# Kernel tuning notes

Hardware: AMD Instinct MI355X
Metric: run time of the kernel (lower is better)

The kernel has to match this reference:

```python
import jax, jax.numpy as jnp
import numpy as np
from jax.scipy.linalg import cho_solve

N, D, K, M = 2048, 128, 8, 64
JITTER = 1e-5


def setup_inputs() -> dict:
    key = jax.random.key(0)
    ks = jax.random.split(key, 5)
    X = jax.random.normal(ks[0], (N, D), jnp.float32)
    Y = jax.random.normal(ks[1], (N, 1), jnp.float32)
    q_mu = 0.1 * jax.random.normal(ks[2], (K, D), jnp.float32)
    # positive variational covariances ~ 1/D, as in the original init
    q_cov = jax.random.uniform(ks[3], (K, D), jnp.float32, 0.5 / D, 1.5 / D)
    Z = jax.random.normal(ks[4], (M, K), jnp.float32)
    sigma_f = jnp.float32(1.0)
    noise_var = jnp.float32(0.01)
    return {"X": X, "Y": Y, "q_mu": q_mu, "q_cov": q_cov, "Z": Z,
            "sigma_f": sigma_f, "noise_var": noise_var}


def _compute_psi1(X, q_mu, q_cov, Z, sigma_f):
    # q_mu_X: (K, N)
    q_mu_X = jnp.einsum('kd,nd->kn', q_mu, X)
    # top: (K, N, M)
    top = (q_mu_X[:, :, None] - Z.T[:, None, :]) ** 2
    # bot: (K, N)
    bot = 1.0 + jnp.einsum('kd,nd->kn', q_cov, X * X)
    bot = bot[:, :, None]
    psi1 = jnp.exp(-0.5 * top / bot) / jnp.sqrt(bot)  # (K, N, M)
    return sigma_f * jnp.prod(psi1, axis=0)  # (N, M)


def _compute_batched_psi2(X, q_mu, q_cov, Z, sigma_f):
    q_mu_X = jnp.einsum('kd,nd->kn', q_mu, X)  # (K, N)
    Z_diff = Z[:, None, :] - Z[None, :, :]      # (M, M, K)
    Z_bar = 0.5 * (Z[:, None, :] + Z[None, :, :])  # (M, M, K)
    # top: (K, N, M, M) -- the dominant intermediate
    top = (q_mu_X[:, :, None, None] - jnp.transpose(Z_bar, (2, 0, 1))[:, None, :, :]) ** 2
    bot = 2.0 * jnp.einsum('kd,nd->kn', q_cov, X * X) + 1.0  # (K, N)
    bot = bot[:, :, None, None]
    right = jnp.prod(jnp.exp(-top / bot) / jnp.sqrt(bot), axis=0)  # (N, M, M)
    left = (sigma_f ** 2) * jnp.exp(-0.25 * jnp.sum(Z_diff ** 2, axis=2))  # (M, M)
    return left * right  # (N, M, M)


def _rbf_K(Z):
    # ARD RBF with unit variance and unit lengthscales (frozen in original)
    sq = jnp.sum((Z[:, None, :] - Z[None, :, :]) ** 2, axis=-1)
    return jnp.exp(-0.5 * sq)


def _chol_logdet(chol):
    return 2.0 * jnp.sum(jnp.log(jnp.diagonal(chol)), axis=-1)


def _elbo(X, Y, q_mu, q_cov, Z, sigma_f, noise_var):
    n = X.shape[0]
    d = X.shape[1]
    m = Z.shape[0]
    sigma2 = jnp.reshape(noise_var, ())
    sf = jnp.reshape(sigma_f, ())
    two_pi = jnp.asarray(2.0 * np.pi, X.dtype)
    eye = jnp.eye(m, dtype=X.dtype)

    Kuu = _rbf_K(Z) + eye * JITTER
    chol_Ku = jnp.linalg.cholesky(Kuu)
    F1 = -n * jnp.log(two_pi) - (n - m) * jnp.log(sigma2) + _chol_logdet(chol_Ku)

    YY = Y.T @ Y  # (1, 1)
    psi2 = jnp.sum(_compute_batched_psi2(X, q_mu, q_cov, Z, sf), axis=0)  # (M, M)
    Ku_Psi2 = sigma2 * Kuu + psi2 + eye * JITTER
    chol_Ku_Psi2 = jnp.linalg.cholesky(Ku_Psi2)
    F1 = F1 - _chol_logdet(chol_Ku_Psi2) - YY / sigma2  # (1, 1)

    psi1 = _compute_psi1(X, q_mu, q_cov, Z, sf)  # (N, M)
    Psi1_Y = psi1.T @ Y  # (M, 1)
    F1 = F1 + (Psi1_Y.T @ cho_solve((chol_Ku_Psi2, True), Psi1_Y)) / sigma2

    psi0 = n * sf ** 2
    KuiPsi2 = cho_solve((chol_Ku, True), psi2)
    F1 = F1 - psi0 / sigma2 + jnp.trace(KuiPsi2) / sigma2

    KL = jnp.sum(jnp.log(q_cov), axis=1)
    KL = KL - d * jnp.log(jnp.sum(q_cov + q_mu ** 2, axis=1))
    KL = KL + d * jnp.asarray(np.log(d), X.dtype)
    KL = jnp.sum(KL)
    return jnp.squeeze(0.5 * (F1 + KL))


def reference(X, Y, q_mu, q_cov, Z, sigma_f, noise_var):
    return _elbo(X, Y, q_mu, q_cov, Z, sigma_f, noise_var)
```

## Files before the change

### kernel.cpp

```cpp
#include <hip/hip_runtime.h>
#include <math.h>

namespace {
constexpr int N_ = 2048;
constexpr int D_ = 128;
constexpr int K_ = 8;
constexpr int M_ = 64;
constexpr float JIT = 1e-5f;
constexpr float L2E = 1.4426950408889634f;
constexpr float LN2 = 0.6931471805599453f;

constexpr int OFF_ARR2 = 16;
constexpr int OFF_C2   = OFF_ARR2 + N_ * 16;
constexpr int OFF_ARR1 = OFF_C2 + N_;
constexpr int OFF_CY   = OFF_ARR1 + N_ * 16;
constexpr int OFF_P2P  = OFF_CY + N_;
constexpr int OFF_P1Y  = OFF_P2P + 16 * 4096;
constexpr int OFF_PSI2 = OFF_P1Y + 512;
constexpr int OFF_KUI  = OFF_PSI2 + 4096;
constexpr int OFF_SC   = OFF_KUI + 4096;
}

struct F8 { float f[8]; };

__device__ __forceinline__ void bar_arrive(int* c) {
  __syncthreads();
  if (threadIdx.x == 0) { __threadfence(); atomicAdd(c, 1); }
}
__device__ __forceinline__ void bar_wait(int* c, int target) {
  if (threadIdx.x == 0) {
    while (__hip_atomic_load(c, __ATOMIC_RELAXED, __HIP_MEMORY_SCOPE_AGENT) < target)
      __builtin_amdgcn_s_sleep(16);
    __threadfence();
  }
  __syncthreads();
}

__device__ __forceinline__ float sweep2x2_w4(
    float* reg, float (*rowbuf)[2][M_], int wave, int lane) {
  float ld = 0.f;
#pragma unroll
  for (int p = 0; p < M_; p += 2) {
    const int par = (p >> 1) & 1;
    float* rbA = rowbuf[par][0];
    float* rbB = rowbuf[par][1];
    const int rp = p & 15;
    if (wave == (p >> 4)) {
      rbA[lane] = reg[rp];
      rbB[lane] = reg[rp + 1];
    }
    __syncthreads();

    const float P00 = rbA[p];
    const float P01 = rbA[p + 1];
    const float P11 = rbB[p + 1];
    const float a0  = rbA[lane];
    const float a1  = rbB[lane];
    const float det = fmaf(P00, P11, -P01 * P01);
    const float idet = __builtin_amdgcn_rcpf(det);
    ld += __log2f(det);
    const float Pi00 =  P11 * idet;
    const float Pi01 = -P01 * idet;
    const float Pi11 =  P00 * idet;

    const bool isp = (lane == p), isq = (lane == p + 1);
    const float w0 = isp ? Pi00 : (isq ? Pi01 : fmaf(Pi00, a0, Pi01 * a1));
    const float w1 = isp ? Pi01 : (isq ? Pi11 : fmaf(Pi01, a0, Pi11 * a1));
    const float t0 = isp ? (1.f - w0) : (isq ? -w0 : w0);
    const float t1 = isq ? (1.f - w1) : (isp ? -w1 : w1);
    const float f0 = (isp || isq) ? -w0 : w0;
    const float f1 = (isp || isq) ? -w1 : w1;

    const float4* rAq = reinterpret_cast<const float4*>(rbA + 16 * wave);
    const float4* rBq = reinterpret_cast<const float4*>(rbB + 16 * wave);
#pragma unroll
    for (int q = 0; q < 4; q++) {
      const float4 va = rAq[q], vb = rBq[q];
      reg[4 * q + 0] = fmaf(-t1, vb.x, fmaf(-t0, va.x, reg[4 * q + 0]));
      reg[4 * q + 1] = fmaf(-t1, vb.y, fmaf(-t0, va.y, reg[4 * q + 1]));
      reg[4 * q + 2] = fmaf(-t1, vb.z, fmaf(-t0, va.z, reg[4 * q + 2]));
      reg[4 * q + 3] = fmaf(-t1, vb.w, fmaf(-t0, va.w, reg[4 * q + 3]));
    }
    if (wave == (p >> 4)) {
      reg[rp]     = f0;
      reg[rp + 1] = f1;
    }
  }
  return ld;
}

__global__ __launch_bounds__(256) void vdmgp_k1(
    const float* __restrict__ X, const float* __restrict__ Y,
    const float* __restrict__ qmu, const float* __restrict__ qcov,
    const float* __restrict__ Z, float* __restrict__ ws) {
  __shared__ float smu[D_ * K_];
  __shared__ float scov[D_ * K_];
  __shared__ float zl[M_][9];
  __shared__ __align__(16) float rowbuf[2][2][M_];
  const int tid = threadIdx.x;
  const int b = blockIdx.x;

  if (b == 0 && tid < 4) ((int*)ws)[tid] = 0;

  if (b == 8) {
    for (int idx = tid; idx < M_ * K_; idx += 256) zl[idx >> 3][idx & 7] = Z[idx];
    __syncthreads();
    const int lane = tid & 63;
    const int wave = tid >> 6;
    float zj[K_];
#pragma unroll
    for (int k = 0; k < K_; k++) zj[k] = zl[lane][k];
    float reg[16];
#pragma unroll
    for (int r = 0; r < 16; r++) {
      const int gi = 16 * wave + r;
      float sq = 0.f;
#pragma unroll
      for (int k = 0; k < K_; k++) { const float dd = zl[gi][k] - zj[k]; sq = fmaf(dd, dd, sq); }
      reg[r] = exp2f(-0.5f * L2E * sq) + ((gi == lane) ? JIT : 0.f);
    }
    const float ld1 = sweep2x2_w4(reg, rowbuf, wave, lane);
#pragma unroll
    for (int r = 0; r < 16; r++)
      ws[OFF_KUI + (16 * wave + r) * 64 + lane] = reg[r];
    if (tid == 0) ws[OFF_SC + 2] = LN2 * ld1;
    return;
  }

  if (b == 9) {
    const int lane = tid & 63;
    const int wave = tid >> 6;
    if (wave == 0) {
      float yy = 0.f;
#pragma unroll
      for (int t = 0; t < 32; t++) {
        const float y = Y[t * 64 + lane];
        yy = fmaf(y, y, yy);
      }
#pragma unroll
      for (int off = 32; off > 0; off >>= 1) yy += __shfl_down(yy, off, 64);
      if (lane == 0) ws[OFF_SC + 0] = yy;
    } else if (wave == 1) {
      const int k = lane >> 3;
      const int d0 = (lane & 7) * 16;
      float slog = 0.f, srow = 0.f;
#pragma unroll
      for (int t = 0; t < 16; t++) {
        const float qc = qcov[k * D_ + d0 + t];
        const float qm = qmu[k * D_ + d0 + t];
        slog += logf(qc);
        srow += qc + qm * qm;
      }
#pragma unroll
      for (int off = 4; off > 0; off >>= 1) {
        slog += __shfl_down(slog, off, 8);
        srow += __shfl_down(srow, off, 8);
      }
      float klr = ((lane & 7) == 0)
          ? (slog - (float)D_ * logf(srow) + (float)D_ * logf((float)D_)) : 0.f;
      klr += __shfl_down(klr, 32, 64);
      klr += __shfl_down(klr, 16, 64);
      klr += __shfl_down(klr, 8, 64);
      if (lane == 0) ws[OFF_SC + 1] = klr;
    }
    return;
  }

  for (int idx = tid; idx < K_ * D_; idx += 256) {
    int k = idx >> 7, d = idx & 127;
    smu[d * K_ + k]  = qmu[idx];
    scov[d * K_ + k] = qcov[idx];
  }
  __syncthreads();

  const int n = b * 256 + tid;
  float a[K_], s2[K_];
#pragma unroll
  for (int k = 0; k < K_; k++) { a[k] = 0.f; s2[k] = 0.f; }

  const float4* xrow = reinterpret_cast<const float4*>(X + n * D_);
#pragma unroll 2
  for (int dq = 0; dq < D_ / 4; dq++) {
    float4 xv = xrow[dq];
    float xs[4] = {xv.x, xv.y, xv.z, xv.w};
#pragma unroll
    for (int t = 0; t < 4; t++) {
      const int d = dq * 4 + t;
      const float x = xs[t];
      const float xx = x * x;
      F8 mu = *reinterpret_cast<const F8*>(&smu[d * K_]);
      F8 cv = *reinterpret_cast<const F8*>(&scov[d * K_]);
#pragma unroll
      for (int k = 0; k < K_; k++) {
        a[k]  = fmaf(mu.f[k], x, a[k]);
        s2[k] = fmaf(cv.f[k], xx, s2[k]);
      }
    }
  }

  float4 w2[4], w1[4];
  float prod2 = 1.f, prod1 = 1.f;
#pragma unroll
  for (int k = 0; k < K_; k++) {
    const float b2 = 2.f * s2[k] + 1.f;
    const float b1 = 1.f + s2[k];
    reinterpret_cast<float*>(w2)[k]     = a[k];
    reinterpret_cast<float*>(w2)[8 + k] = L2E / b2;
    reinterpret_cast<float*>(w1)[k]     = a[k];
    reinterpret_cast<float*>(w1)[8 + k] = 0.5f * L2E / b1;
    prod2 *= rsqrtf(b2);
    prod1 *= rsqrtf(b1);
  }
  float4* a2q = reinterpret_cast<float4*>(ws + OFF_ARR2 + n * 16);
  float4* a1q = reinterpret_cast<float4*>(ws + OFF_ARR1 + n * 16);
#pragma unroll
  for (int e = 0; e < 4; e++) { a2q[e] = w2[e]; a1q[e] = w1[e]; }
  (ws + OFF_C2)[n] = prod2;
  (ws + OFF_CY)[n] = prod1 * Y[n];
}

__global__ __launch_bounds__(256) void vdmgp_k2(
    const float* __restrict__ Z,
    const float* __restrict__ sfp, const float* __restrict__ nvp,
    float* __restrict__ ws, float* __restrict__ out) {
  __shared__ __align__(16) float pool[5520];

  int* bar = (int*)ws;
  const int tid = threadIdx.x;
  const int b = blockIdx.x;
  const float sf = sfp[0];

  if (b > 0) {
    const int t = b - 1;
    {
      float* sa = pool;
      float* sc = pool + 2048;
      const int chunk = t >> 4;
      const int nbase = chunk * 128;
      const float4* src = reinterpret_cast<const float4*>(ws + OFF_ARR2 + nbase * 16);
      float4* dst = reinterpret_cast<float4*>(sa);
      for (int idx = tid; idx < 128 * 4; idx += 256) dst[idx] = src[idx];
      if (tid < 128) sc[tid] = (ws + OFF_C2)[nbase + tid];
      __syncthreads();

      const int pair = (t & 15) * 256 + tid;
      const int i = pair >> 6, j = pair & 63;
      float zb[K_];
#pragma unroll
      for (int k = 0; k < K_; k++) zb[k] = 0.5f * (Z[i * K_ + k] + Z[j * K_ + k]);

      float acc = 0.f;
      for (int nl = 0; nl < 128; nl++) {
        const F8 av = *reinterpret_cast<const F8*>(&sa[nl * 16]);
        const F8 ib = *reinterpret_cast<const F8*>(&sa[nl * 16 + 8]);
        float s = 0.f;
#pragma unroll
        for (int k = 0; k < K_; k++) {
          const float tt = av.f[k] - zb[k];
          s = fmaf(tt * tt, ib.f[k], s);
        }
        acc = fmaf(sc[nl], exp2f(-s), acc);
      }
      (ws + OFF_P2P)[chunk * 4096 + pair] = acc;
    }
    bar_arrive(&bar[0]);

    if (t < 16) {
      bar_wait(&bar[0], 256);
      const int p = t * 256 + tid;
      float acc = 0.f;
#pragma unroll
      for (int c = 0; c < 16; c++) acc += ws[OFF_P2P + c * 4096 + p];
      const int i = p >> 6, j = p & 63;
      float sq = 0.f;
#pragma unroll
      for (int k = 0; k < K_; k++) {
        const float dd = Z[i * K_ + k] - Z[j * K_ + k];
        sq = fmaf(dd, dd, sq);
      }
      ws[OFF_PSI2 + p] = sf * sf * exp2f(-0.25f * L2E * sq) * acc;
      bar_arrive(&bar[2]);
    } else if (t < 24) {
      float* sa1 = pool;
      float* scy = pool + 4096;
      float* red = pool + 4352;
      const int chunk = t - 16;
      const int nbase = chunk * 256;
      const float4* src = reinterpret_cast<const float4*>(ws + OFF_ARR1 + nbase * 16);
      float4* dst = reinterpret_cast<float4*>(sa1);
#pragma unroll
      for (int r = 0; r < 4; r++) dst[r * 256 + tid] = src[r * 256 + tid];
      scy[tid] = (ws + OFF_CY)[nbase + tid];
      __syncthreads();

      const int m = tid & 63;
      const int stripe = tid >> 6;
      float zm[K_];
#pragma unroll
      for (int k = 0; k < K_; k++) zm[k] = Z[m * K_ + k];

      float acc = 0.f;
      for (int u = 0; u < 64; u++) {
        const int nl = stripe * 64 + u;
        const F8 av = *reinterpret_cast<const F8*>(&sa1[nl * 16]);
        const F8 ib = *reinterpret_cast<const F8*>(&sa1[nl * 16 + 8]);
        float s = 0.f;
#pragma unroll
        for (int k = 0; k < K_; k++) {
          const float d = av.f[k] - zm[k];
          s = fmaf(d * d, ib.f[k], s);
        }
        acc = fmaf(scy[nl], exp2f(-s), acc);
      }
      red[tid] = acc;
      __syncthreads();
      if (tid < 64)
        (ws + OFF_P1Y)[chunk * 64 + tid] =
            red[tid] + red[64 + tid] + red[128 + tid] + red[192 + tid];
      bar_arrive(&bar[1]);
    }
    return;
  }

  float (*P2s)[M_]       = reinterpret_cast<float(*)[M_]>(pool);
  float (*zl)[9]         = reinterpret_cast<float(*)[9]>(pool + 4096);
  float (*rowbuf)[2][M_] = reinterpret_cast<float(*)[2][M_]>(pool + 4672);
  float* pysL  = pool + 4928;
  float* scalL = pool + 4992;
  float* redQ  = pool + 5000;
  float* redT  = pool + 5256;

  const int lane = tid & 63;
  const int wave = tid >> 6;
  const float s2v = nvp[0];

  for (int idx = tid; idx < M_ * K_; idx += 256) zl[idx >> 3][idx & 7] = Z[idx];

  bar_wait(&bar[2], 16);
  {
    const float4* srcq = reinterpret_cast<const float4*>(ws + OFF_PSI2);
    float4* dstq = reinterpret_cast<float4*>(&P2s[0][0]);
#pragma unroll
    for (int q = 0; q < 4; q++) dstq[q * 256 + tid] = srcq[q * 256 + tid];
  }
  bar_wait(&bar[1], 8);
  if (tid < M_) {
    float s = 0.f;
#pragma unroll
    for (int c = 0; c < 8; c++) s += ws[OFF_P1Y + c * M_ + tid];
    pysL[tid] = sf * s;
  }
  __syncthreads();

  float zj[K_];
#pragma unroll
  for (int k = 0; k < K_; k++) zj[k] = zl[lane][k];
  float reg[16];
#pragma unroll
  for (int r = 0; r < 16; r++) {
    const int gi = 16 * wave + r;
    float sq = 0.f;
#pragma unroll
    for (int k = 0; k < K_; k++) { const float dd = zl[gi][k] - zj[k]; sq = fmaf(dd, dd, sq); }
    const float jit = (gi == lane) ? JIT : 0.f;
    const float kj = exp2f(-0.5f * L2E * sq) + jit;
    reg[r] = fmaf(s2v, kj, P2s[gi][lane] + jit);
  }

  const float ld2 = sweep2x2_w4(reg, rowbuf, wave, lane);

  float sQ = 0.f, sT = 0.f;
  const float* kui = ws + OFF_KUI;
#pragma unroll
  for (int r = 0; r < 16; r++) {
    const int gi = 16 * wave + r;
    sQ = fmaf(reg[r], pysL[gi], sQ);
    sT = fmaf(kui[gi * 64 + lane], P2s[gi][lane], sT);
  }
  redQ[tid] = sQ;
  redT[tid] = sT;
  if (tid == 0) scalL[6] = LN2 * ld2;
  __syncthreads();

  if (wave == 0) {
    float c = redQ[lane] + redQ[64 + lane] + redQ[128 + lane] + redQ[192 + lane];
    float q = c * pysL[lane];
#pragma unroll
    for (int off = 32; off > 0; off >>= 1) q += __shfl_down(q, off, 64);
    if (lane == 0) scalL[7] = -q;
  } else if (wave == 1) {
    float s = redT[lane] + redT[64 + lane] + redT[128 + lane] + redT[192 + lane];
#pragma unroll
    for (int off = 32; off > 0; off >>= 1) s += __shfl_down(s, off, 64);
    if (lane == 0) scalL[5] = -s;
  }
  __syncthreads();

  if (tid == 0) {
    const float YY  = ws[OFF_SC + 0];
    const float KL  = ws[OFF_SC + 1];
    const float ld1 = ws[OFF_SC + 2];
    const float tr = scalL[5], ld2v = scalL[6], quad = scalL[7];
    const float inv = 1.0f / s2v;
    const float F1 = -(float)N_ * 1.8378770664093453f
                   - (float)(N_ - M_) * logf(s2v)
                   + (ld1 - ld2v)
                   - YY * inv
                   + quad * inv
                   - (float)N_ * sf * sf * inv
                   + tr * inv;
    out[0] = 0.5f * (F1 + KL);
  }
}

extern "C" void kernel_launch(void* const* d_in, const int* in_sizes, int n_in,
                              void* d_out, int out_size, void* d_ws, size_t ws_size,
                              hipStream_t stream) {
  const float* X    = (const float*)d_in[0];
  const float* Y    = (const float*)d_in[1];
  const float* qmu  = (const float*)d_in[2];
  const float* qcov = (const float*)d_in[3];
  const float* Z    = (const float*)d_in[4];
  const float* sfp  = (const float*)d_in[5];
  const float* nvp  = (const float*)d_in[6];
  float* ws  = (float*)d_ws;
  float* out = (float*)d_out;

  vdmgp_k1<<<10, 256, 0, stream>>>(X, Y, qmu, qcov, Z, ws);
  vdmgp_k2<<<257, 256, 0, stream>>>(Z, sfp, nvp, ws, out);
}
```

Before: 52.51 us.

## Pipeline Cholesky sweep rows, split psi2 barriers, and reorder final-block waits

The 2x2 block sweep now computes the next pivot row pair early and writes it to the alternate row buffer, so each step needs one block barrier instead of two phases. The single global psi2 barrier becomes sixteen per-tile counters, so each reducer block waits only on its own sixteen producers, and the sleep intervals are shorter. The final block does its Kuu and Kui loads before waiting on psi2, reads psi2 straight from global memory instead of staging it in shared memory, and waits for psi1·Y only after the sweep. The psi2 inner loop is unrolled by four to expose more independent exp work, at the cost of more registers.

```diff
diff --git a/kernel.cpp b/kernel.cpp
--- a/kernel.cpp
+++ b/kernel.cpp
@@ -10,7 +10,7 @@
 constexpr float L2E = 1.4426950408889634f;
 constexpr float LN2 = 0.6931471805599453f;
 
-constexpr int OFF_ARR2 = 16;
+constexpr int OFF_ARR2 = 32;
 constexpr int OFF_C2   = OFF_ARR2 + N_ * 16;
 constexpr int OFF_ARR1 = OFF_C2 + N_;
 constexpr int OFF_CY   = OFF_ARR1 + N_ * 16;
@@ -27,29 +27,34 @@
   __syncthreads();
   if (threadIdx.x == 0) { __threadfence(); atomicAdd(c, 1); }
 }
+template <int SLP>
 __device__ __forceinline__ void bar_wait(int* c, int target) {
   if (threadIdx.x == 0) {
     while (__hip_atomic_load(c, __ATOMIC_RELAXED, __HIP_MEMORY_SCOPE_AGENT) < target)
-      __builtin_amdgcn_s_sleep(16);
+      __builtin_amdgcn_s_sleep(SLP);
     __threadfence();
   }
   __syncthreads();
 }
 
-__device__ __forceinline__ float sweep2x2_w4(
+__device__ __forceinline__ float sweep2x2_pipe(
     float* reg, float (*rowbuf)[2][M_], int wave, int lane) {
+  if (wave == 0) {
+    rowbuf[0][0][lane] = reg[0];
+    rowbuf[0][1][lane] = reg[1];
+  }
+  __syncthreads();
   float ld = 0.f;
 #pragma unroll
-  for (int p = 0; p < M_; p += 2) {
-    const int par = (p >> 1) & 1;
+  for (int s = 0; s < 32; ++s) {
+    const int p = 2 * s;
+    const int par = s & 1;
     float* rbA = rowbuf[par][0];
     float* rbB = rowbuf[par][1];
-    const int rp = p & 15;
-    if (wave == (p >> 4)) {
-      rbA[lane] = reg[rp];
-      rbB[lane] = reg[rp + 1];
-    }
-    __syncthreads();
+    const int own_s  = s >> 3;
+    const int own_s1 = (s + 1) >> 3;
+    const int rp  = p & 15;
+    const int rp2 = (p + 2) & 15;
 
     const float P00 = rbA[p];
     const float P01 = rbA[p + 1];
@@ -71,6 +76,13 @@
     const float f0 = (isp || isq) ? -w0 : w0;
     const float f1 = (isp || isq) ? -w1 : w1;
 
+    if (s < 31 && wave == own_s1) {
+      const float e0 = fmaf(-t1, rbB[p + 2], fmaf(-t0, rbA[p + 2], reg[rp2]));
+      const float e1 = fmaf(-t1, rbB[p + 3], fmaf(-t0, rbA[p + 3], reg[rp2 + 1]));
+      rowbuf[par ^ 1][0][lane] = e0;
+      rowbuf[par ^ 1][1][lane] = e1;
+    }
+
     const float4* rAq = reinterpret_cast<const float4*>(rbA + 16 * wave);
     const float4* rBq = reinterpret_cast<const float4*>(rbB + 16 * wave);
 #pragma unroll
@@ -81,10 +93,8 @@
       reg[4 * q + 2] = fmaf(-t1, vb.z, fmaf(-t0, va.z, reg[4 * q + 2]));
       reg[4 * q + 3] = fmaf(-t1, vb.w, fmaf(-t0, va.w, reg[4 * q + 3]));
     }
-    if (wave == (p >> 4)) {
-      reg[rp]     = f0;
-      reg[rp + 1] = f1;
-    }
+    if (wave == own_s) { reg[rp] = f0; reg[rp + 1] = f1; }
+    __syncthreads();
   }
   return ld;
 }
@@ -100,7 +110,7 @@
   const int tid = threadIdx.x;
   const int b = blockIdx.x;
 
-  if (b == 0 && tid < 4) ((int*)ws)[tid] = 0;
+  if (b == 0 && tid < 32) ((int*)ws)[tid] = 0;
 
   if (b == 8) {
     for (int idx = tid; idx < M_ * K_; idx += 256) zl[idx >> 3][idx & 7] = Z[idx];
@@ -119,7 +129,7 @@
       for (int k = 0; k < K_; k++) { const float dd = zl[gi][k] - zj[k]; sq = fmaf(dd, dd, sq); }
       reg[r] = exp2f(-0.5f * L2E * sq) + ((gi == lane) ? JIT : 0.f);
     }
-    const float ld1 = sweep2x2_w4(reg, rowbuf, wave, lane);
+    const float ld1 = sweep2x2_pipe(reg, rowbuf, wave, lane);
 #pragma unroll
     for (int r = 0; r < 16; r++)
       ws[OFF_KUI + (16 * wave + r) * 64 + lane] = reg[r];
@@ -223,7 +233,7 @@
     const float* __restrict__ Z,
     const float* __restrict__ sfp, const float* __restrict__ nvp,
     float* __restrict__ ws, float* __restrict__ out) {
-  __shared__ __align__(16) float pool[5520];
+  __shared__ __align__(16) float pool[4864];
 
   int* bar = (int*)ws;
   const int tid = threadIdx.x;
@@ -250,23 +260,34 @@
       for (int k = 0; k < K_; k++) zb[k] = 0.5f * (Z[i * K_ + k] + Z[j * K_ + k]);
 
       float acc = 0.f;
-      for (int nl = 0; nl < 128; nl++) {
-        const F8 av = *reinterpret_cast<const F8*>(&sa[nl * 16]);
-        const F8 ib = *reinterpret_cast<const F8*>(&sa[nl * 16 + 8]);
-        float s = 0.f;
+      for (int nl = 0; nl < 128; nl += 4) {
+        F8 av0 = *reinterpret_cast<const F8*>(&sa[(nl + 0) * 16]);
+        F8 ib0 = *reinterpret_cast<const F8*>(&sa[(nl + 0) * 16 + 8]);
+        F8 av1 = *reinterpret_cast<const F8*>(&sa[(nl + 1) * 16]);
+        F8 ib1 = *reinterpret_cast<const F8*>(&sa[(nl + 1) * 16 + 8]);
+        F8 av2 = *reinterpret_cast<const F8*>(&sa[(nl + 2) * 16]);
+        F8 ib2 = *reinterpret_cast<const F8*>(&sa[(nl + 2) * 16 + 8]);
+        F8 av3 = *reinterpret_cast<const F8*>(&sa[(nl + 3) * 16]);
+        F8 ib3 = *reinterpret_cast<const F8*>(&sa[(nl + 3) * 16 + 8]);
+        float s0 = 0.f, s1 = 0.f, s2 = 0.f, s3 = 0.f;
 #pragma unroll
         for (int k = 0; k < K_; k++) {
-          const float tt = av.f[k] - zb[k];
-          s = fmaf(tt * tt, ib.f[k], s);
+          const float d0 = av0.f[k] - zb[k]; s0 = fmaf(d0 * d0, ib0.f[k], s0);
+          const float d1 = av1.f[k] - zb[k]; s1 = fmaf(d1 * d1, ib1.f[k], s1);
+          const float d2 = av2.f[k] - zb[k]; s2 = fmaf(d2 * d2, ib2.f[k], s2);
+          const float d3 = av3.f[k] - zb[k]; s3 = fmaf(d3 * d3, ib3.f[k], s3);
         }
-        acc = fmaf(sc[nl], exp2f(-s), acc);
-      }
-      (ws + OFF_P2P)[chunk * 4096 + pair] = acc;
-    }
-    bar_arrive(&bar[0]);
+        acc = fmaf(sc[nl + 0], exp2f(-s0), acc);
+        acc = fmaf(sc[nl + 1], exp2f(-s1), acc);
+        acc = fmaf(sc[nl + 2], exp2f(-s2), acc);
+        acc = fmaf(sc[nl + 3], exp2f(-s3), acc);
+      }
+      (ws + OFF_P2P)[chunk * 4096 + (t & 15) * 256 + tid] = acc;
+    }
+    bar_arrive(&bar[t & 15]);
 
     if (t < 16) {
-      bar_wait(&bar[0], 256);
+      bar_wait<4>(&bar[t], 16);
       const int p = t * 256 + tid;
       float acc = 0.f;
 #pragma unroll
@@ -279,7 +300,7 @@
         sq = fmaf(dd, dd, sq);
       }
       ws[OFF_PSI2 + p] = sf * sf * exp2f(-0.25f * L2E * sq) * acc;
-      bar_arrive(&bar[2]);
+      bar_arrive(&bar[17]);
     } else if (t < 24) {
       float* sa1 = pool;
       float* scy = pool + 4096;
@@ -317,45 +338,29 @@
       if (tid < 64)
         (ws + OFF_P1Y)[chunk * 64 + tid] =
             red[tid] + red[64 + tid] + red[128 + tid] + red[192 + tid];
-      bar_arrive(&bar[1]);
+      bar_arrive(&bar[16]);
     }
     return;
   }
 
-  float (*P2s)[M_]       = reinterpret_cast<float(*)[M_]>(pool);
-  float (*zl)[9]         = reinterpret_cast<float(*)[9]>(pool + 4096);
-  float (*rowbuf)[2][M_] = reinterpret_cast<float(*)[2][M_]>(pool + 4672);
-  float* pysL  = pool + 4928;
-  float* scalL = pool + 4992;
-  float* redQ  = pool + 5000;
-  float* redT  = pool + 5256;
+  float (*zl)[9]         = reinterpret_cast<float(*)[9]>(pool);
+  float (*rowbuf)[2][M_] = reinterpret_cast<float(*)[2][M_]>(pool + 576);
+  float* pysL  = pool + 832;
+  float* scalL = pool + 896;
+  float* redQ  = pool + 912;
+  float* redT  = pool + 1168;
 
   const int lane = tid & 63;
   const int wave = tid >> 6;
   const float s2v = nvp[0];
 
   for (int idx = tid; idx < M_ * K_; idx += 256) zl[idx >> 3][idx & 7] = Z[idx];
-
-  bar_wait(&bar[2], 16);
-  {
-    const float4* srcq = reinterpret_cast<const float4*>(ws + OFF_PSI2);
-    float4* dstq = reinterpret_cast<float4*>(&P2s[0][0]);
-#pragma unroll
-    for (int q = 0; q < 4; q++) dstq[q * 256 + tid] = srcq[q * 256 + tid];
-  }
-  bar_wait(&bar[1], 8);
-  if (tid < M_) {
-    float s = 0.f;
-#pragma unroll
-    for (int c = 0; c < 8; c++) s += ws[OFF_P1Y + c * M_ + tid];
-    pysL[tid] = sf * s;
-  }
   __syncthreads();
 
   float zj[K_];
 #pragma unroll
   for (int k = 0; k < K_; k++) zj[k] = zl[lane][k];
-  float reg[16];
+  float base[16], kui16[16];
 #pragma unroll
   for (int r = 0; r < 16; r++) {
     const int gi = 16 * wave + r;
@@ -363,23 +368,38 @@
 #pragma unroll
     for (int k = 0; k < K_; k++) { const float dd = zl[gi][k] - zj[k]; sq = fmaf(dd, dd, sq); }
     const float jit = (gi == lane) ? JIT : 0.f;
-    const float kj = exp2f(-0.5f * L2E * sq) + jit;
-    reg[r] = fmaf(s2v, kj, P2s[gi][lane] + jit);
-  }
-
-  const float ld2 = sweep2x2_w4(reg, rowbuf, wave, lane);
-
-  float sQ = 0.f, sT = 0.f;
-  const float* kui = ws + OFF_KUI;
+    base[r] = fmaf(s2v, exp2f(-0.5f * L2E * sq) + jit, jit);
+    kui16[r] = ws[OFF_KUI + gi * 64 + lane];
+  }
+
+  bar_wait<2>(&bar[17], 16);
+
+  float reg[16];
+  float sT = 0.f;
 #pragma unroll
   for (int r = 0; r < 16; r++) {
     const int gi = 16 * wave + r;
-    sQ = fmaf(reg[r], pysL[gi], sQ);
-    sT = fmaf(kui[gi * 64 + lane], P2s[gi][lane], sT);
-  }
+    const float p2v = ws[OFF_PSI2 + gi * 64 + lane];
+    reg[r] = base[r] + p2v;
+    sT = fmaf(kui16[r], p2v, sT);
+  }
+  redT[tid] = sT;
+
+  const float ld2 = sweep2x2_pipe(reg, rowbuf, wave, lane);
+
+  bar_wait<2>(&bar[16], 8);
+  if (tid < M_) {
+    float s = 0.f;
+#pragma unroll
+    for (int c = 0; c < 8; c++) s += ws[OFF_P1Y + c * M_ + tid];
+    pysL[tid] = sf * s;
+  }
+  __syncthreads();
+
+  float sQ = 0.f;
+#pragma unroll
+  for (int r = 0; r < 16; r++) sQ = fmaf(reg[r], pysL[16 * wave + r], sQ);
   redQ[tid] = sQ;
-  redT[tid] = sT;
-  if (tid == 0) scalL[6] = LN2 * ld2;
   __syncthreads();
 
   if (wave == 0) {
@@ -400,11 +420,11 @@
     const float YY  = ws[OFF_SC + 0];
     const float KL  = ws[OFF_SC + 1];
     const float ld1 = ws[OFF_SC + 2];
-    const float tr = scalL[5], ld2v = scalL[6], quad = scalL[7];
+    const float tr = scalL[5], quad = scalL[7];
     const float inv = 1.0f / s2v;
     const float F1 = -(float)N_ * 1.8378770664093453f
                    - (float)(N_ - M_) * logf(s2v)
-                   + (ld1 - ld2v)
+                   + (ld1 - LN2 * ld2)
                    - YY * inv
                    + quad * inv
                    - (float)N_ * sf * sf * inv
```

New measurement: 50.00 us, median of 2. 4.8% less time.
